# Kernel optimization log

Measured on AMD Instinct MI355X. Metric: run time of the kernel, lower is better.

Reference implementation:

```python
import jax, jax.numpy as jnp
import numpy as np

EPS = 1e-5

def _c1(W, x, b=None):
    # 1x1 conv on (B,C,J,T)
    y = jnp.einsum('oc,bcjt->bojt', W, x)
    if b is not None:
        y = y + b[None, :, None, None]
    return y

def _c1s(W, x, b=None):
    # 1x1 conv on batch-free (C,J,T)
    y = jnp.einsum('oc,cjt->ojt', W, x)
    if b is not None:
        y = y + b[:, None, None]
    return y

def _bn(x, p):
    # eval-mode batchnorm; p is (4,C) = gamma, beta, running_mean, running_var
    g, b, m, v = p[0], p[1], p[2], p[3]
    shp = (1, -1) + (1,) * (x.ndim - 2)
    inv = g / jnp.sqrt(v + EPS)
    return (x - m.reshape(shp)) * inv.reshape(shp) + b.reshape(shp)

def _adaptive_max_w(x, out_w):
    # AdaptiveMaxPool over last dim of (B,C,W) -> (B,C,out_w), torch bin rule
    W = x.shape[-1]
    cols = []
    for i in range(out_w):
        s = (i * W) // out_w
        e = -((-(i + 1) * W) // out_w)
        cols.append(jnp.max(x[..., s:e], axis=-1))
    return jnp.stack(cols, axis=-1)

def _gcn(x1, g, w, w1, b1, bnp):
    # gcn_spa: y[b,c,j,t] = sum_k g[b,t,j,k] * x1[b,c,k,t]
    y = jnp.einsum('btjk,bckt->bcjt', g, x1)
    out = _c1(w, y) + _c1(w1, x1, b1)
    return jax.nn.relu(_bn(out, bnp))

def setup_inputs() -> dict:
    key = jax.random.key(0)
    B, J, T = 4, 224, 224
    specs = {
        'x': (B, 3, J, T),
        'je1_w': (64, 3), 'je1_b': (64,), 'je2_w': (64, 64), 'je2_b': (64,),
        'se1_w': (64, J), 'se1_b': (64,), 'se2_w': (64, 64), 'se2_b': (64,),
        'te1_w': (64, T), 'te1_b': (64,), 'te2_w': (256, 64), 'te2_b': (256,),
        'g1_w': (256, 128), 'g1_b': (256,), 'g2_w': (256, 128), 'g2_b': (256,),
        'gcn1_w': (128, 128), 'gcn1_w1': (128, 128), 'gcn1_b': (128,),
        'gcn2_w': (256, 128), 'gcn2_w1': (256, 128), 'gcn2_b': (256,),
        'gcn3_w': (256, 256), 'gcn3_w1': (256, 256), 'gcn3_b': (256,),
        'loc1_w': (256, 256, 1, 3), 'loc1_b': (256,),
        'loc2_w': (512, 256), 'loc2_b': (512,),
    }
    bns = {'bn0': 672, 'gcn1_bn': 128, 'gcn2_bn': 256,
           'gcn3_bn': 256, 'loc1_bn': 256, 'loc2_bn': 512}
    out = {}
    for i, (name, shp) in enumerate(specs.items()):
        k = jax.random.fold_in(key, i)
        scale = 1.0 if name == 'x' else 0.1
        out[name] = jax.random.normal(k, shp, dtype=jnp.float32) * scale
    for i, (name, c) in enumerate(bns.items()):
        k = jax.random.fold_in(key, 100 + i)
        out[name] = jax.random.uniform(k, (4, c), dtype=jnp.float32)
    return out

def reference(x, bn0, je1_w, je1_b, je2_w, je2_b, se1_w, se1_b, se2_w, se2_b,
              te1_w, te1_b, te2_w, te2_b, g1_w, g1_b, g2_w, g2_b,
              gcn1_w, gcn1_w1, gcn1_b, gcn1_bn,
              gcn2_w, gcn2_w1, gcn2_b, gcn2_bn,
              gcn3_w, gcn3_w1, gcn3_b, gcn3_bn,
              loc1_w, loc1_b, loc1_bn, loc2_w, loc2_b, loc2_bn):
    bs, c, J, T = x.shape
    eye = jnp.eye(J, dtype=x.dtype)
    # spa one-hot after permute: [c,j,t] = delta_cj; tem: [c,j,t] = delta_ct
    spa_oh = jnp.broadcast_to(eye[:, :, None], (J, J, T))
    tem_oh = jnp.broadcast_to(eye[:, None, :], (T, J, T))
    # embeds of constant one-hots (identical across batch)
    tem1 = jax.nn.relu(_c1s(te2_w, jax.nn.relu(_c1s(te1_w, tem_oh, te1_b)), te2_b))  # (256,J,T)
    spa1 = jax.nn.relu(_c1s(se2_w, jax.nn.relu(_c1s(se1_w, spa_oh, se1_b)), se2_b))  # (64,J,T)
    # joint_embed with norm_data_custom (BN1d over flattened c*J channels)
    xf = _bn(x.reshape(bs, c * J, T), bn0).reshape(bs, c, J, T)
    pos = jax.nn.relu(_c1(je2_w, jax.nn.relu(_c1(je1_w, xf, je1_b)), je2_b))  # (bs,64,J,T)
    h = jnp.concatenate([pos, jnp.broadcast_to(spa1[None], (bs,) + spa1.shape)], axis=1)  # (bs,128,J,T)
    # compute_g_spa: per-timestep joint affinity with softmax
    q = _c1(g1_w, h, g1_b)  # (bs,256,J,T)
    k = _c1(g2_w, h, g2_b)
    g = jax.nn.softmax(jnp.einsum('bcjt,bckt->btjk', q, k), axis=-1)  # (bs,T,J,J)
    h = _gcn(h, g, gcn1_w, gcn1_w1, gcn1_b, gcn1_bn)
    h = _gcn(h, g, gcn2_w, gcn2_w1, gcn2_b, gcn2_bn)
    h = _gcn(h, g, gcn3_w, gcn3_w1, gcn3_b, gcn3_bn)
    h = h + tem1[None]
    # local: AdaptiveMaxPool2d((1,20)) then temporal conv k=(1,3) pad=(0,1)
    h = jnp.max(h, axis=2)           # (bs,256,T)
    h = _adaptive_max_w(h, 20)       # (bs,256,20)
    h = h[:, :, None, :]             # (bs,256,1,20)
    h = jax.lax.conv_general_dilated(h, loc1_w, (1, 1), ((0, 0), (1, 1)),
                                     dimension_numbers=('NCHW', 'OIHW', 'NCHW'))
    h = jax.nn.relu(_bn(h + loc1_b[None, :, None, None], loc1_bn))
    # dropout2d is identity in eval mode
    h = jax.nn.relu(_bn(_c1(loc2_w, h, loc2_b), loc2_bn))
    return jnp.max(h, axis=(2, 3), keepdims=True)  # (bs,512,1,1)
```

## Files before the change

kernel.cpp:

```cpp
#include <hip/hip_runtime.h>
#include <hip/hip_bf16.h>

typedef __hip_bfloat16 bf16;
typedef __attribute__((ext_vector_type(8))) short v8s;
typedef __attribute__((ext_vector_type(4))) float f32x4;
#define EPS 1e-5f
#define MFMA16(a, b, c) __builtin_amdgcn_mfma_f32_16x16x32_bf16(a, b, c, 0, 0, 0)

__device__ __forceinline__ float bfu(unsigned int s) {
  union { unsigned int u; float f; } c; c.u = s << 16; return c.f;
}
__device__ __forceinline__ bf16 f2b(float v) { return __float2bfloat16(v); }

__global__ __launch_bounds__(256) void k_small(
    const float* __restrict__ te1_w, const float* __restrict__ te1_b,
    const float* __restrict__ te2_w, const float* __restrict__ te2_b,
    const float* __restrict__ se1_w, const float* __restrict__ se1_b,
    const float* __restrict__ se2_w, const float* __restrict__ se2_b,
    float* __restrict__ tem1, bf16* __restrict__ spa1T) {
  int idx = blockIdx.x * 256 + threadIdx.x;
  if (idx >= (256 + 64) * 224) return;
  int o = idx / 224, t = idx % 224;
  if (o < 256) {
    float acc = te2_b[o];
    for (int c = 0; c < 64; ++c) {
      float u = fmaxf(te1_w[c * 224 + t] + te1_b[c], 0.f);
      acc += te2_w[o * 64 + c] * u;
    }
    tem1[o * 224 + t] = fmaxf(acc, 0.f);
  } else {
    int oo = o - 256;
    float acc = se2_b[oo];
    for (int c = 0; c < 64; ++c) {
      float u = fmaxf(se1_w[c * 224 + t] + se1_b[c], 0.f);
      acc += se2_w[oo * 64 + c] * u;
    }
    spa1T[t * 64 + oo] = f2b(fmaxf(acc, 0.f));
  }
}

__global__ __launch_bounds__(256) void k_wm(
    const float* __restrict__ g1_w, const float* __restrict__ g2_w,
    const float* __restrict__ g1_b, bf16* __restrict__ WmH, bf16* __restrict__ WmL,
    float* __restrict__ dvec) {
  int idx = blockIdx.x * 256 + threadIdx.x;
  if (idx >= 128 * 128) return;
  int o = idx >> 7, c = idx & 127;
  float acc = 0.f;
  for (int t = 0; t < 256; ++t) acc += g1_w[t * 128 + c] * g2_w[t * 128 + o];
  bf16 hi = f2b(acc);
  WmH[o * 128 + c] = hi;
  WmL[o * 128 + c] = f2b(acc - __bfloat162float(hi));
  if (c == 0) {
    float d = 0.f;
    for (int t = 0; t < 256; ++t) d += g2_w[t * 128 + o] * g1_b[t];
    dvec[o] = d;
  }
}

__global__ __launch_bounds__(256) void k_wcvt(
    const float* __restrict__ g1w, const float* __restrict__ g1w1,
    const float* __restrict__ g2w, const float* __restrict__ g2w1,
    const float* __restrict__ g3w, const float* __restrict__ g3w1,
    const float* __restrict__ je2w, bf16* __restrict__ dst) {
  int idx = blockIdx.x * 256 + threadIdx.x;
  const float* src; size_t base; int off;
  if (idx < 16384)        { src = g1w;  base = 0;      off = idx;          }
  else if (idx < 32768)   { src = g1w1; base = 16384;  off = idx - 16384;  }
  else if (idx < 65536)   { src = g2w;  base = 32768;  off = idx - 32768;  }
  else if (idx < 98304)   { src = g2w1; base = 65536;  off = idx - 65536;  }
  else if (idx < 163840)  { src = g3w;  base = 98304;  off = idx - 98304;  }
  else if (idx < 229376)  { src = g3w1; base = 163840; off = idx - 163840; }
  else if (idx < 233472)  {
    int off2 = idx - 229376;
    float v = je2w[off2];
    bf16 hi = f2b(v);
    dst[229376 + off2] = hi;
    dst[233472 + off2] = f2b(v - __bfloat162float(hi));
    return;
  }
  else return;
  dst[base + off] = f2b(src[off]);
}

__global__ __launch_bounds__(256, 2) void k_h0_mfma(
    const float* __restrict__ x, const float* __restrict__ bn0,
    const float* __restrict__ je1_w, const float* __restrict__ je1_b,
    const bf16* __restrict__ je2wb, const float* __restrict__ je2_b,
    const bf16* __restrict__ spa1T, bf16* __restrict__ H0) {
  __shared__ bf16 Uh[2 * 7168];
  __shared__ bf16 Ul[2 * 7168];
  __shared__ bf16 Wh[2 * 2048];
  __shared__ bf16 Wl[2 * 2048];
  __shared__ float w1s[192], b1s[64];
  const int bt = blockIdx.x;
  const int b = bt / 224, t = bt - b * 224;
  const int tid = threadIdx.x;
  if (tid < 192) w1s[tid] = je1_w[tid];
  if (tid < 64) b1s[tid] = je1_b[tid];
  #pragma unroll
  for (int sh = 0; sh < 2; ++sh) {
    int idx = sh * 256 + tid;
    int kt = idx >> 8, rem = idx & 255;
    int o = rem >> 2, qq = rem & 3;
    v8s wh = *(const v8s*)(je2wb + o * 64 + kt * 32 + qq * 8);
    v8s wl = *(const v8s*)(je2wb + 4096 + o * 64 + kt * 32 + qq * 8);
    *(v8s*)(Wh + kt * 2048 + (o * 4 + qq) * 8) = wh;
    *(v8s*)(Wl + kt * 2048 + (o * 4 + qq) * 8) = wl;
  }
  __syncthreads();
  if (tid < 224) {
    const int j = tid;
    float xf[3];
    #pragma unroll
    for (int c = 0; c < 3; ++c) {
      int ch = c * 224 + j;
      float g = bn0[ch], bb = bn0[672 + ch], m = bn0[1344 + ch], v = bn0[2016 + ch];
      float inv = g * rsqrtf(v + EPS);
      float xv = x[((size_t)(b * 3 + c) * 224 + j) * 224 + t];
      xf[c] = (xv - m) * inv + bb;
    }
    float u[64];
    #pragma unroll
    for (int c = 0; c < 64; ++c) {
      float a = w1s[c * 3] * xf[0] + w1s[c * 3 + 1] * xf[1] + w1s[c * 3 + 2] * xf[2] + b1s[c];
      u[c] = fmaxf(a, 0.f);
    }
    #pragma unroll
    for (int kt = 0; kt < 2; ++kt)
      #pragma unroll
      for (int qq = 0; qq < 4; ++qq) {
        unsigned int ph[4], pl[4];
        #pragma unroll
        for (int e = 0; e < 4; ++e) {
          float v0 = u[kt * 32 + qq * 8 + 2 * e];
          float v1 = u[kt * 32 + qq * 8 + 2 * e + 1];
          bf16 h0 = f2b(v0), h1 = f2b(v1);
          bf16 l0 = f2b(v0 - __bfloat162float(h0));
          bf16 l1 = f2b(v1 - __bfloat162float(h1));
          ph[e] = (unsigned int)__bfloat16_as_ushort(h0) |
                  ((unsigned int)__bfloat16_as_ushort(h1) << 16);
          pl[e] = (unsigned int)__bfloat16_as_ushort(l0) |
                  ((unsigned int)__bfloat16_as_ushort(l1) << 16);
        }
        *(uint4*)(Uh + kt * 7168 + (j * 4 + qq) * 8) = make_uint4(ph[0], ph[1], ph[2], ph[3]);
        *(uint4*)(Ul + kt * 7168 + (j * 4 + qq) * 8) = make_uint4(pl[0], pl[1], pl[2], pl[3]);
      }
    const uint4* sp = (const uint4*)(spa1T + j * 64);
    uint4* dp = (uint4*)(H0 + ((size_t)bt * 224 + j) * 128 + 64);
    #pragma unroll
    for (int i = 0; i < 8; ++i) dp[i] = sp[i];
  }
  __syncthreads();
  const int w = tid >> 6, lane = tid & 63;
  const int l15 = lane & 15, q = lane >> 4;
  for (int mt = w; mt < 14; mt += 4) {
    v8s ah[2], al[2];
    #pragma unroll
    for (int kt = 0; kt < 2; ++kt) {
      ah[kt] = *(const v8s*)(Uh + kt * 7168 + ((mt * 16 + l15) * 4 + q) * 8);
      al[kt] = *(const v8s*)(Ul + kt * 7168 + ((mt * 16 + l15) * 4 + q) * 8);
    }
    #pragma unroll
    for (int nt = 0; nt < 4; ++nt) {
      f32x4 acc = {0.f, 0.f, 0.f, 0.f};
      #pragma unroll
      for (int kt = 0; kt < 2; ++kt) {
        v8s bh = *(const v8s*)(Wh + kt * 2048 + ((nt * 16 + l15) * 4 + q) * 8);
        v8s bl = *(const v8s*)(Wl + kt * 2048 + ((nt * 16 + l15) * 4 + q) * 8);
        acc = MFMA16(ah[kt], bl, acc);
        acc = MFMA16(al[kt], bh, acc);
        acc = MFMA16(ah[kt], bh, acc);
      }
      const int oc = nt * 16 + l15;
      const float bi = je2_b[oc];
      #pragma unroll
      for (int r = 0; r < 4; ++r) {
        size_t m = (size_t)bt * 224 + mt * 16 + q * 4 + r;
        H0[m * 128 + oc] = f2b(fmaxf(acc[r] + bi, 0.f));
      }
    }
  }
}

template <int CIN, int COUT, int DUAL, int WLO, int WRITE_T>
__global__ __launch_bounds__(512, 4) void k_conv_mfma(
    const bf16* __restrict__ in1,
    const bf16* __restrict__ w1h, const bf16* __restrict__ w1l,
    const bf16* __restrict__ in2,
    const bf16* __restrict__ w2h, const bf16* __restrict__ w2l,
    const float* __restrict__ bias, const float* __restrict__ bn,
    int do_relu, bf16* __restrict__ out, bf16* __restrict__ out_t) {
  constexpr int HALF = CIN / 32;
  constexpr int NST = (1 + DUAL) * HALF;
  constexpr int TSZ = 4096;
  constexpr int NT = 2 + WLO;
  __shared__ bf16 smem[2 * NT * TSZ];
  const int tid = threadIdx.x;
  const int w = tid >> 6, lane = tid & 63;
  const int l15 = lane & 15, q = lane >> 4;
  const int mh = w >> 2, nq = w & 3;
  const int m0 = blockIdx.x * 128;
  const int n0blk = blockIdx.y * 128;
  const int n0w = n0blk + nq * 32;
  const int crow = tid >> 2;
  const int ckp = tid & 3;

  f32x4 acc[4][2] = {};
  v8s TA, TH, TL;

  auto gload = [&](int s) {
    const bool second = DUAL && (s >= HALF);
    const bf16* ia = second ? in2 : in1;
    const bf16* wh = second ? w2h : w1h;
    const int kk = (second ? s - HALF : s) * 32 + ckp * 8;
    TA = *(const v8s*)(ia + (size_t)(m0 + crow) * CIN + kk);
    TH = *(const v8s*)(wh + (size_t)(n0blk + crow) * CIN + kk);
    if (WLO) {
      const bf16* wl = second ? w2l : w1l;
      TL = *(const v8s*)(wl + (size_t)(n0blk + crow) * CIN + kk);
    }
  };
  auto swrite = [&](int buf) {
    bf16* b = smem + buf * NT * TSZ;
    *(v8s*)(b + tid * 8) = TA;
    *(v8s*)(b + TSZ + tid * 8) = TH;
    if (WLO) *(v8s*)(b + 2 * TSZ + tid * 8) = TL;
  };

  gload(0);
  swrite(0);
  for (int s = 0; s < NST; ++s) {
    __syncthreads();
    if (s + 1 < NST) gload(s + 1);
    const bf16* base = smem + (s & 1) * NT * TSZ;
    v8s a[4];
    #pragma unroll
    for (int i = 0; i < 4; ++i) {
      const int row = mh * 64 + i * 16 + l15;
      a[i] = *(const v8s*)(base + (row * 4 + q) * 8);
    }
    #pragma unroll
    for (int ns = 0; ns < 2; ++ns) {
      const int ncol = nq * 32 + ns * 16 + l15;
      v8s bh = *(const v8s*)(base + TSZ + (ncol * 4 + q) * 8);
      if (WLO) {
        v8s bl = *(const v8s*)(base + 2 * TSZ + (ncol * 4 + q) * 8);
        #pragma unroll
        for (int i = 0; i < 4; ++i) acc[i][ns] = MFMA16(a[i], bl, acc[i][ns]);
      }
      #pragma unroll
      for (int i = 0; i < 4; ++i) acc[i][ns] = MFMA16(a[i], bh, acc[i][ns]);
    }
    if (s + 1 < NST) swrite((s + 1) & 1);
  }
  #pragma unroll
  for (int ns = 0; ns < 2; ++ns) {
    const int oc = n0w + ns * 16 + l15;
    float sc = 1.f, sh = bias[oc];
    if (bn != nullptr) {
      float g = bn[oc], bb = bn[COUT + oc], m = bn[2 * COUT + oc], v = bn[3 * COUT + oc];
      sc = g * rsqrtf(v + EPS);
      sh = (sh - m) * sc + bb;
    }
    #pragma unroll
    for (int i = 0; i < 4; ++i) {
      const int mbase = m0 + mh * 64 + i * 16 + q * 4;
      float vals[4];
      #pragma unroll
      for (int r = 0; r < 4; ++r) {
        float val = acc[i][ns][r] * sc + sh;
        if (do_relu) val = fmaxf(val, 0.f);
        vals[r] = val;
        out[(size_t)(mbase + r) * COUT + oc] = f2b(val);
      }
      if (WRITE_T) {
        const int bt = mbase / 224;
        const int j = mbase - bt * 224;
        unsigned short s0 = __bfloat16_as_ushort(f2b(vals[0]));
        unsigned short s1 = __bfloat16_as_ushort(f2b(vals[1]));
        unsigned short s2 = __bfloat16_as_ushort(f2b(vals[2]));
        unsigned short s3 = __bfloat16_as_ushort(f2b(vals[3]));
        uint2 pk;
        pk.x = (unsigned int)s0 | ((unsigned int)s1 << 16);
        pk.y = (unsigned int)s2 | ((unsigned int)s3 << 16);
        *(uint2*)((unsigned short*)out_t + ((size_t)bt * COUT + oc) * 224 + j) = pk;
      }
    }
  }
}

__global__ __launch_bounds__(256) void k_transpose128(
    const bf16* __restrict__ src, bf16* __restrict__ dst) {
  const int j0 = blockIdx.x * 32, c0 = blockIdx.y * 32, bt = blockIdx.z;
  __shared__ unsigned short ts[32][33];
  const int tid = threadIdx.x;
  {
    int r = tid >> 3, cg = (tid & 7) * 4;
    const unsigned short* sp =
        (const unsigned short*)src + ((size_t)(bt * 224) + j0 + r) * 128 + c0 + cg;
    uint2 u = *(const uint2*)sp;
    ts[r][cg + 0] = (unsigned short)(u.x & 0xffffu);
    ts[r][cg + 1] = (unsigned short)(u.x >> 16);
    ts[r][cg + 2] = (unsigned short)(u.y & 0xffffu);
    ts[r][cg + 3] = (unsigned short)(u.y >> 16);
  }
  __syncthreads();
  {
    int c = tid >> 3, jg = (tid & 7) * 4;
    uint2 o;
    o.x = (unsigned int)ts[jg + 0][c] | ((unsigned int)ts[jg + 1][c] << 16);
    o.y = (unsigned int)ts[jg + 2][c] | ((unsigned int)ts[jg + 3][c] << 16);
    *(uint2*)((unsigned short*)dst + ((size_t)(bt * 128) + c0 + c) * 224 + j0 + jg) = o;
  }
}

__global__ __launch_bounds__(256, 3) void k_scores_mfma(
    const bf16* __restrict__ A, const bf16* __restrict__ H, bf16* __restrict__ G) {
  const int bid = blockIdx.x;
  const int xcd = bid & 7, slot = bid >> 3;
  const int mtg = slot & 3, bt = (slot >> 2) * 8 + xcd;
  const int w = threadIdx.x >> 6, lane = threadIdx.x & 63;
  const int mt = mtg * 4 + w;
  if (mt >= 14) return;
  const int l15 = lane & 15, q = lane >> 4;
  const int j0 = mt * 16;
  const bf16* Ab = A + (size_t)bt * 224 * 128;
  const bf16* Hb = H + (size_t)bt * 224 * 128;
  v8s a[4];
  #pragma unroll
  for (int ks = 0; ks < 4; ++ks)
    a[ks] = *(const v8s*)(Ab + (size_t)(j0 + l15) * 128 + ks * 32 + q * 8);
  f32x4 s[14];
  #pragma unroll
  for (int nt = 0; nt < 14; ++nt) {
    f32x4 acc = {0.f, 0.f, 0.f, 0.f};
    #pragma unroll
    for (int ks = 0; ks < 4; ++ks) {
      v8s b = *(const v8s*)(Hb + (size_t)(nt * 16 + l15) * 128 + ks * 32 + q * 8);
      acc = MFMA16(a[ks], b, acc);
    }
    s[nt] = acc;
  }
  bf16* Gb = G + ((size_t)bt * 224 + j0) * 224;
  #pragma unroll
  for (int r = 0; r < 4; ++r) {
    float mx = -1e30f;
    #pragma unroll
    for (int nt = 0; nt < 14; ++nt) mx = fmaxf(mx, s[nt][r]);
    mx = fmaxf(mx, __shfl_xor(mx, 1));
    mx = fmaxf(mx, __shfl_xor(mx, 2));
    mx = fmaxf(mx, __shfl_xor(mx, 4));
    mx = fmaxf(mx, __shfl_xor(mx, 8));
    float sum = 0.f;
    #pragma unroll
    for (int nt = 0; nt < 14; ++nt) {
      float e = __expf(s[nt][r] - mx);
      s[nt][r] = e;
      sum += e;
    }
    sum += __shfl_xor(sum, 1);
    sum += __shfl_xor(sum, 2);
    sum += __shfl_xor(sum, 4);
    sum += __shfl_xor(sum, 8);
    const float inv = 1.f / sum;
    const int jr = q * 4 + r;
    #pragma unroll
    for (int nt = 0; nt < 14; ++nt)
      Gb[(size_t)jr * 224 + nt * 16 + l15] = f2b(s[nt][r] * inv);
  }
}

template <int C>
__global__ __launch_bounds__(256, 3) void k_apply_mfma(
    const bf16* __restrict__ G, const bf16* __restrict__ Ht,
    bf16* __restrict__ Y) {
  const int bid = blockIdx.x;
  const int xcd = bid & 7, slot = bid >> 3;
  const int jt = slot % 7, bt = (slot / 7) * 8 + xcd;
  const int w = threadIdx.x >> 6;
  const int lane = threadIdx.x & 63;
  const int l15 = lane & 15, q = lane >> 4;
  const int j0 = jt * 32;
  const bf16* Gb = G + (size_t)bt * 224 * 224;
  const bf16* Hb = Ht + (size_t)bt * C * 224;
  bf16* Yb = Y + (size_t)bt * 224 * C;
  v8s a[2][7];
  #pragma unroll
  for (int h = 0; h < 2; ++h)
    #pragma unroll
    for (int ks = 0; ks < 7; ++ks)
      a[h][ks] = *(const v8s*)(Gb + (size_t)(j0 + h * 16 + l15) * 224 + ks * 32 + q * 8);
  constexpr int NPW = C / 64;
  #pragma unroll
  for (int u = 0; u < NPW; ++u) {
    const int nt = w * NPW + u;
    f32x4 acc0 = {0.f, 0.f, 0.f, 0.f};
    f32x4 acc1 = {0.f, 0.f, 0.f, 0.f};
    #pragma unroll
    for (int ks = 0; ks < 7; ++ks) {
      v8s b = *(const v8s*)(Hb + (size_t)(nt * 16 + l15) * 224 + ks * 32 + q * 8);
      acc0 = MFMA16(a[0][ks], b, acc0);
      acc1 = MFMA16(a[1][ks], b, acc1);
    }
    const int c = nt * 16 + l15;
    #pragma unroll
    for (int r = 0; r < 4; ++r) {
      Yb[(size_t)(j0 + q * 4 + r) * C + c] = f2b(acc0[r]);
      Yb[(size_t)(j0 + 16 + q * 4 + r) * C + c] = f2b(acc1[r]);
    }
  }
}

__global__ __launch_bounds__(256) void k_reduce(
    const bf16* __restrict__ H3, float* __restrict__ Hred, int row0) {
  int t = blockIdx.x;
  int jb = blockIdx.y;
  int o = threadIdx.x;
  const unsigned short* p =
      (const unsigned short*)(H3 + ((size_t)t * 224 + jb * 32) * 256 + o);
  float mx = 0.f;
  #pragma unroll 8
  for (int j = 0; j < 32; ++j) mx = fmaxf(mx, bfu(p[(size_t)j * 256]));
  atomicMax((unsigned int*)&Hred[(size_t)(row0 + t) * 256 + o], __float_as_uint(mx));
}

__global__ __launch_bounds__(256) void k_head_a(
    const float* __restrict__ Hred, const float* __restrict__ tem1,
    float* __restrict__ Hm) {
  int b = blockIdx.x, i = blockIdx.y, c = threadIdx.x;
  int s = (i * 224) / 20, e = ((i + 1) * 224 + 19) / 20;
  float mx = -1e30f;
  for (int t = s; t < e; ++t)
    mx = fmaxf(mx, Hred[((size_t)b * 224 + t) * 256 + c] + tem1[c * 224 + t]);
  Hm[((size_t)b * 20 + i) * 256 + c] = mx;
}

__global__ __launch_bounds__(256) void k_head_b(
    const float* __restrict__ Hm, const float* __restrict__ loc1_w,
    const float* __restrict__ loc1_b, const float* __restrict__ loc1_bn,
    float* __restrict__ Z1) {
  int b = blockIdx.x, r = blockIdx.y;
  __shared__ float hs[3 * 256];
  int tid = threadIdx.x;
  for (int idx = tid; idx < 768; idx += 256) {
    int dx = idx >> 8, c = idx & 255;
    int u = r + dx - 1;
    hs[idx] = (u >= 0 && u < 20) ? Hm[((size_t)b * 20 + u) * 256 + c] : 0.f;
  }
  __syncthreads();
  int o = tid;
  float acc = loc1_b[o];
  const float* wp = loc1_w + (size_t)o * 768;
  #pragma unroll 4
  for (int c = 0; c < 256; ++c) {
    acc += wp[c * 3 + 0] * hs[c] + wp[c * 3 + 1] * hs[256 + c] + wp[c * 3 + 2] * hs[512 + c];
  }
  float g = loc1_bn[o], bb = loc1_bn[256 + o], m = loc1_bn[512 + o], v = loc1_bn[768 + o];
  float sc = g * rsqrtf(v + EPS);
  Z1[((size_t)b * 20 + r) * 256 + o] = fmaxf((acc - m) * sc + bb, 0.f);
}

__global__ __launch_bounds__(512) void k_head_c(
    const float* __restrict__ Z1, const float* __restrict__ loc2_w,
    const float* __restrict__ loc2_b, const float* __restrict__ loc2_bn,
    float* __restrict__ out) {
  int b = blockIdx.x;
  int tid = threadIdx.x;
  __shared__ float zs[20 * 256];
  for (int idx = tid; idx < 5120; idx += 512) zs[idx] = Z1[(size_t)b * 5120 + idx];
  __syncthreads();
  int o2 = tid;
  float acc[20];
  float bi = loc2_b[o2];
  #pragma unroll
  for (int r = 0; r < 20; ++r) acc[r] = bi;
  const float* wp = loc2_w + (size_t)o2 * 256;
  for (int c = 0; c < 256; ++c) {
    float wv = wp[c];
    #pragma unroll
    for (int r = 0; r < 20; ++r) acc[r] += wv * zs[r * 256 + c];
  }
  float g = loc2_bn[o2], bb = loc2_bn[512 + o2], m = loc2_bn[1024 + o2], v = loc2_bn[1536 + o2];
  float sc = g * rsqrtf(v + EPS);
  float best = -1e30f;
  #pragma unroll
  for (int r = 0; r < 20; ++r) best = fmaxf(best, fmaxf((acc[r] - m) * sc + bb, 0.f));
  out[(size_t)b * 512 + o2] = best;
}

extern "C" void kernel_launch(void* const* d_in, const int* in_sizes, int n_in,
                              void* d_out, int out_size, void* d_ws, size_t ws_size,
                              hipStream_t stream) {
  const float* x       = (const float*)d_in[0];
  const float* je1_w   = (const float*)d_in[1];
  const float* je1_b   = (const float*)d_in[2];
  const float* je2_w   = (const float*)d_in[3];
  const float* je2_b   = (const float*)d_in[4];
  const float* se1_w   = (const float*)d_in[5];
  const float* se1_b   = (const float*)d_in[6];
  const float* se2_w   = (const float*)d_in[7];
  const float* se2_b   = (const float*)d_in[8];
  const float* te1_w   = (const float*)d_in[9];
  const float* te1_b   = (const float*)d_in[10];
  const float* te2_w   = (const float*)d_in[11];
  const float* te2_b   = (const float*)d_in[12];
  const float* g1_w    = (const float*)d_in[13];
  const float* g1_b    = (const float*)d_in[14];
  const float* g2_w    = (const float*)d_in[15];
  const float* gcn1_w  = (const float*)d_in[17];
  const float* gcn1_w1 = (const float*)d_in[18];
  const float* gcn1_b  = (const float*)d_in[19];
  const float* gcn2_w  = (const float*)d_in[20];
  const float* gcn2_w1 = (const float*)d_in[21];
  const float* gcn2_b  = (const float*)d_in[22];
  const float* gcn3_w  = (const float*)d_in[23];
  const float* gcn3_w1 = (const float*)d_in[24];
  const float* gcn3_b  = (const float*)d_in[25];
  const float* loc1_w  = (const float*)d_in[26];
  const float* loc1_b  = (const float*)d_in[27];
  const float* loc2_w  = (const float*)d_in[28];
  const float* loc2_b  = (const float*)d_in[29];
  const float* bn0     = (const float*)d_in[30];
  const float* gcn1_bn = (const float*)d_in[31];
  const float* gcn2_bn = (const float*)d_in[32];
  const float* gcn3_bn = (const float*)d_in[33];
  const float* loc1_bn = (const float*)d_in[34];
  const float* loc2_bn = (const float*)d_in[35];
  float* out = (float*)d_out;
  (void)in_sizes; (void)n_in; (void)out_size; (void)ws_size;

  char* ws = (char*)d_ws;
  size_t off = 0;
  auto take = [&](size_t bytes) -> char* {
    char* p = ws + off;
    off += (bytes + 255) & ~(size_t)255;
    return p;
  };
  const size_t M  = 200704;
  const size_t Mc = 50176;
  float* tem1  = (float*)take(256 * 224 * 4);
  bf16* spa1T  = (bf16*)take(224 * 64 * 2);
  bf16* WmH    = (bf16*)take(128 * 128 * 2);
  bf16* WmL    = (bf16*)take(128 * 128 * 2);
  float* dvec  = (float*)take(128 * 4);
  bf16* wb     = (bf16*)take(237568 * 2);
  float* Hm    = (float*)take(4 * 20 * 256 * 4);
  float* Z1    = (float*)take(4 * 20 * 256 * 4);
  float* Hred  = (float*)take(896 * 256 * 4);
  bf16* H0    = (bf16*)take(M * 128 * 2);
  bf16* Afull = (bf16*)take(M * 128 * 2);
  bf16* YZ  = (bf16*)take(Mc * 256 * 2);
  bf16* Wb  = (bf16*)take(Mc * 256 * 2);
  bf16* HtV = (bf16*)take(Mc * 256 * 2);
  bf16* Gm  = (bf16*)take(Mc * 224 * 2);
  bf16* Yr = YZ;
  bf16* Zr = YZ + Mc * 128;

  bf16* g1w_h  = wb;
  bf16* g1w1_h = wb + 16384;
  bf16* g2w_h  = wb + 32768;
  bf16* g2w1_h = wb + 65536;
  bf16* g3w_h  = wb + 98304;
  bf16* g3w1_h = wb + 163840;
  bf16* je2wb  = wb + 229376;

  hipMemsetAsync(Hred, 0, 896 * 256 * 4, stream);
  k_small<<<280, 256, 0, stream>>>(te1_w, te1_b, te2_w, te2_b,
                                   se1_w, se1_b, se2_w, se2_b, tem1, spa1T);
  k_wm<<<64, 256, 0, stream>>>(g1_w, g2_w, g1_b, WmH, WmL, dvec);
  k_wcvt<<<912, 256, 0, stream>>>(gcn1_w, gcn1_w1, gcn2_w, gcn2_w1,
                                  gcn3_w, gcn3_w1, je2_w, wb);
  k_h0_mfma<<<896, 256, 0, stream>>>(x, bn0, je1_w, je1_b, je2wb, je2_b, spa1T, H0);

  k_conv_mfma<128, 128, 0, 1, 0><<<dim3(1568, 1), 512, 0, stream>>>(
      H0, WmH, WmL, nullptr, nullptr, nullptr, dvec, nullptr, 0, Afull, nullptr);

  for (int b = 0; b < 4; ++b) {
    const bf16* H0c = H0 + (size_t)b * Mc * 128;
    const bf16* Ac  = Afull + (size_t)b * Mc * 128;
    k_transpose128<<<dim3(7, 4, 224), 256, 0, stream>>>(H0c, HtV);
    k_scores_mfma<<<896, 256, 0, stream>>>(Ac, H0c, Gm);
    k_apply_mfma<128><<<1568, 256, 0, stream>>>(Gm, HtV, Yr);
    k_conv_mfma<128, 128, 1, 0, 1><<<dim3(392, 1), 512, 0, stream>>>(
        Yr, g1w_h, nullptr, H0c, g1w1_h, nullptr, gcn1_b, gcn1_bn, 1, Zr, HtV);
    k_apply_mfma<128><<<1568, 256, 0, stream>>>(Gm, HtV, Yr);
    k_conv_mfma<128, 256, 1, 0, 1><<<dim3(392, 2), 512, 0, stream>>>(
        Yr, g2w_h, nullptr, Zr, g2w1_h, nullptr, gcn2_b, gcn2_bn, 1, Wb, HtV);
    k_apply_mfma<256><<<1568, 256, 0, stream>>>(Gm, HtV, YZ);
    k_conv_mfma<256, 256, 1, 0, 0><<<dim3(392, 2), 512, 0, stream>>>(
        YZ, g3w_h, nullptr, Wb, g3w1_h, nullptr, gcn3_b, gcn3_bn, 1, HtV, nullptr);
    k_reduce<<<dim3(224, 7), 256, 0, stream>>>(HtV, Hred, b * 224);
  }
  k_head_a<<<dim3(4, 20), 256, 0, stream>>>(Hred, tem1, Hm);
  k_head_b<<<dim3(4, 20), 256, 0, stream>>>(Hm, loc1_w, loc1_b, loc1_bn, Z1);
  k_head_c<<<4, 512, 0, stream>>>(Z1, loc2_w, loc2_b, loc2_bn, out);
}
```

Before: 974.0 us.

## Stage G and H tiles through LDS with double-buffered prefetch in apply kernel

```diff
diff --git a/kernel.cpp b/kernel.cpp
--- a/kernel.cpp
+++ b/kernel.cpp
@@ -372,43 +372,72 @@
 }
 
 template <int C>
-__global__ __launch_bounds__(256, 3) void k_apply_mfma(
+__global__ __launch_bounds__(256, 2) void k_apply_mfma(
     const bf16* __restrict__ G, const bf16* __restrict__ Ht,
     bf16* __restrict__ Y) {
+  constexpr int NST = C / 64;
+  __shared__ bf16 Gs[7168];
+  __shared__ bf16 Ht2[2 * 14336];
   const int bid = blockIdx.x;
   const int xcd = bid & 7, slot = bid >> 3;
   const int jt = slot % 7, bt = (slot / 7) * 8 + xcd;
-  const int w = threadIdx.x >> 6;
-  const int lane = threadIdx.x & 63;
+  const int tid = threadIdx.x;
+  const int w = tid >> 6, lane = tid & 63;
   const int l15 = lane & 15, q = lane >> 4;
   const int j0 = jt * 32;
   const bf16* Gb = G + (size_t)bt * 224 * 224;
   const bf16* Hb = Ht + (size_t)bt * C * 224;
   bf16* Yb = Y + (size_t)bt * 224 * C;
-  v8s a[2][7];
-  #pragma unroll
-  for (int h = 0; h < 2; ++h)
-    #pragma unroll
-    for (int ks = 0; ks < 7; ++ks)
-      a[h][ks] = *(const v8s*)(Gb + (size_t)(j0 + h * 16 + l15) * 224 + ks * 32 + q * 8);
-  constexpr int NPW = C / 64;
-  #pragma unroll
-  for (int u = 0; u < NPW; ++u) {
-    const int nt = w * NPW + u;
+  #pragma unroll
+  for (int it = 0; it < 4; ++it) {
+    int c = it * 256 + tid;
+    if (c < 896)
+      *(v8s*)(Gs + c * 8) = *(const v8s*)(Gb + (size_t)j0 * 224 + c * 8);
+  }
+  v8s T[7];
+  auto gload = [&](int g) {
+    #pragma unroll
+    for (int it = 0; it < 7; ++it) {
+      int c = it * 256 + tid;
+      T[it] = *(const v8s*)(Hb + (size_t)g * 64 * 224 + c * 8);
+    }
+  };
+  auto swrite = [&](int buf) {
+    bf16* bp = Ht2 + buf * 14336;
+    #pragma unroll
+    for (int it = 0; it < 7; ++it) {
+      int c = it * 256 + tid;
+      *(v8s*)(bp + c * 8) = T[it];
+    }
+  };
+  gload(0);
+  swrite(0);
+  __syncthreads();
+  v8s a0[7], a1[7];
+  #pragma unroll
+  for (int ks = 0; ks < 7; ++ks) {
+    a0[ks] = *(const v8s*)(Gs + ((size_t)l15 * 28 + ks * 4 + q) * 8);
+    a1[ks] = *(const v8s*)(Gs + ((size_t)(16 + l15) * 28 + ks * 4 + q) * 8);
+  }
+  for (int g = 0; g < NST; ++g) {
+    if (g) __syncthreads();
+    if (g + 1 < NST) gload(g + 1);
+    const bf16* bp = Ht2 + (g & 1) * 14336;
     f32x4 acc0 = {0.f, 0.f, 0.f, 0.f};
     f32x4 acc1 = {0.f, 0.f, 0.f, 0.f};
     #pragma unroll
     for (int ks = 0; ks < 7; ++ks) {
-      v8s b = *(const v8s*)(Hb + (size_t)(nt * 16 + l15) * 224 + ks * 32 + q * 8);
-      acc0 = MFMA16(a[0][ks], b, acc0);
-      acc1 = MFMA16(a[1][ks], b, acc1);
-    }
-    const int c = nt * 16 + l15;
+      v8s b = *(const v8s*)(bp + ((size_t)(w * 16 + l15) * 28 + ks * 4 + q) * 8);
+      acc0 = MFMA16(a0[ks], b, acc0);
+      acc1 = MFMA16(a1[ks], b, acc1);
+    }
+    const int c = g * 64 + w * 16 + l15;
     #pragma unroll
     for (int r = 0; r < 4; ++r) {
       Yb[(size_t)(j0 + q * 4 + r) * C + c] = f2b(acc0[r]);
       Yb[(size_t)(j0 + 16 + q * 4 + r) * C + c] = f2b(acc1[r]);
     }
+    if (g + 1 < NST) swrite((g + 1) & 1);
   }
 }
 
```

After: 932.6 us. -4.2%, faster.
